# Optimization experiments

Hardware: AMD Instinct MI355X
Metric: run time of the kernel (lower is better)

## Reference

```python
import jax, jax.numpy as jnp
import numpy as np

E, D, F, K = 8, 1024, 4096, 2  # num_experts, embed_dim, intermediate_dim, top_k


def new_gelu(x):
    # NewGELUActivation: 0.5*x*(1+tanh(sqrt(2/pi)*(x+0.044715*x^3)))
    c = jnp.sqrt(2.0 / jnp.pi).astype(x.dtype)
    return 0.5 * x * (1.0 + jnp.tanh(c * (x + 0.044715 * x * x * x)))


def setup_inputs() -> dict:
    key = jax.random.key(0)
    ks = jax.random.split(key, 6)
    std = 0.02
    return {
        "hidden_states": jax.random.normal(ks[0], (4, 2048, D), dtype=jnp.float32),
        "gate_w": jax.random.normal(ks[1], (E, D), dtype=jnp.float32) * std,   # Linear(out=E,in=D), no bias
        "w_fc": jax.random.normal(ks[2], (E, F, D), dtype=jnp.float32) * std,  # per-expert c_fc weight [out,in]
        "b_fc": jnp.zeros((E, F), dtype=jnp.float32),
        "w_proj": jax.random.normal(ks[3], (E, D, F), dtype=jnp.float32) * std,
        "b_proj": jnp.zeros((E, D), dtype=jnp.float32),
    }


def reference(hidden_states, gate_w, w_fc, b_fc, w_proj, b_proj):
    B, S, _ = hidden_states.shape
    x = hidden_states.reshape(-1, D)                       # [T, D]
    T = x.shape[0]
    logits = x @ gate_w.T                                  # [T, E]
    topk_vals, topk_idx = jax.lax.top_k(logits, K)         # [T, K]
    topk_w = jax.nn.softmax(topk_vals, axis=-1)            # [T, K]
    # scatter top-k weights into a dense [T, E] sparse-weight matrix
    sparse_w = jnp.zeros((T, E), dtype=x.dtype).at[
        jnp.arange(T)[:, None], topk_idx
    ].set(topk_w)
    # per-expert dense MLP, combined with (mostly-zero) routing weights.
    # Mathematically identical to gather->MLP->scatter in the original
    # (dropout is identity in eval mode).
    out = jnp.zeros_like(x)
    for e in range(E):
        h = new_gelu(x @ w_fc[e].T + b_fc[e])              # [T, F]
        y = h @ w_proj[e].T + b_proj[e]                    # [T, D]
        out = out + y * sparse_w[:, e:e + 1]
    return out.reshape(B, S, D)
```

## Files before the change

### kernel.cpp

```cpp
#include <hip/hip_runtime.h>
#include <hip/hip_bf16.h>

#define E_ 8
#define D_ 1024
#define F_ 4096
#define K_ 2

typedef __attribute__((ext_vector_type(8))) short short8;
typedef __attribute__((ext_vector_type(4))) float f32x4;

__device__ __forceinline__ unsigned f2bf(float f){
  union { __hip_bfloat16 h; unsigned short u; } c;
  c.h = __float2bfloat16(f);
  return (unsigned)c.u;
}

__device__ __forceinline__ float bf2f(unsigned u){
  union { float f; unsigned u; } c;
  c.u = u << 16;
  return c.f;
}

__device__ __forceinline__ float gelu_f(float v){
  const float c0 = 0.7978845608028654f;
  float z = c0 * (v + 0.044715f * v * v * v);
  float e = __expf(2.0f * z);
  float t = 1.0f - 2.0f / (1.0f + e);
  return 0.5f * v * (1.0f + t);
}

__device__ __forceinline__ void gload16(const void* gsrc, void* ldst){
  __builtin_amdgcn_global_load_lds(
      (const __attribute__((address_space(1))) unsigned int*)gsrc,
      (__attribute__((address_space(3))) unsigned int*)ldst, 16, 0, 0);
}

__global__ void gate_kernel(const float* __restrict__ x, const float* __restrict__ gw,
                            int* __restrict__ tidx, float* __restrict__ tw, int T){
  int wid = threadIdx.x >> 6, lane = threadIdx.x & 63;
  int t = blockIdx.x * 4 + wid;
  if (t >= T) return;
  const float* xr = x + (size_t)t * D_;
  double acc[E_];
  #pragma unroll
  for (int e = 0; e < E_; ++e) acc[e] = 0.0;
  #pragma unroll
  for (int j = 0; j < 16; ++j){
    float xv = xr[j*64 + lane];
    #pragma unroll
    for (int e = 0; e < E_; ++e)
      acc[e] += (double)xv * (double)gw[e*D_ + j*64 + lane];
  }
  #pragma unroll
  for (int e = 0; e < E_; ++e){
    #pragma unroll
    for (int off = 32; off >= 1; off >>= 1)
      acc[e] += __shfl_xor(acc[e], off);
  }
  if (lane == 0){
    float l[E_];
    #pragma unroll
    for (int e = 0; e < E_; ++e) l[e] = (float)acc[e];
    int i0 = 0; float v0 = l[0];
    #pragma unroll
    for (int e = 1; e < E_; ++e) if (l[e] > v0){ v0 = l[e]; i0 = e; }
    int i1 = -1; float v1 = -1e30f;
    #pragma unroll
    for (int e = 0; e < E_; ++e) if (e != i0 && l[e] > v1){ v1 = l[e]; i1 = e; }
    float e1 = expf(v1 - v0);
    float s = 1.0f + e1;
    tidx[2*t] = i0; tidx[2*t+1] = i1;
    tw[2*t] = 1.0f / s; tw[2*t+1] = e1 / s;
  }
}

__global__ void slotscan_kernel(const int* __restrict__ tidx, int* __restrict__ counts,
                                int* __restrict__ tokSlot, int nAssign){
  __shared__ int cnt[256][E_];
  __shared__ int wtot[E_][4];
  __shared__ int ebase[E_];
  const int tid = threadIdx.x;
  const int lane = tid & 63, w = tid >> 6;
  const int per = (nAssign + 255) >> 8;
  const int base = tid * per;

  #pragma unroll
  for (int e = 0; e < E_; ++e) cnt[tid][e] = 0;
  for (int j = 0; j < per; ++j){
    int i = base + j;
    if (i < nAssign) cnt[tid][tidx[i]]++;
  }
  int excl[E_];
  #pragma unroll
  for (int e = 0; e < E_; ++e){
    int v = cnt[tid][e];
    int s = v;
    #pragma unroll
    for (int off = 1; off < 64; off <<= 1){
      int u = __shfl_up(s, off);
      if (lane >= off) s += u;
    }
    if (lane == 63) wtot[e][w] = s;
    excl[e] = s - v;
  }
  __syncthreads();
  if (tid == 0){
    int pre = 0;
    #pragma unroll
    for (int e = 0; e < E_; ++e){
      int tot = 0;
      #pragma unroll
      for (int ww = 0; ww < 4; ++ww){ int c = wtot[e][ww]; wtot[e][ww] = tot; tot += c; }
      counts[e] = tot;
      ebase[e] = pre;
      pre += (tot + 127) & ~127;
    }
  }
  __syncthreads();
  #pragma unroll
  for (int e = 0; e < E_; ++e)
    cnt[tid][e] = ebase[e] + wtot[e][w] + excl[e];
  for (int j = 0; j < per; ++j){
    int i = base + j;
    if (i < nAssign){
      int e = tidx[i];
      tokSlot[i] = cnt[tid][e]++;
    }
  }
}

__global__ void scatgath_kernel(const float* __restrict__ x,
                                const int* __restrict__ tokSlot,
                                __hip_bfloat16* __restrict__ Abuf){
  int t = blockIdx.x;
  int s0 = tokSlot[K_*t], s1 = tokSlot[K_*t + 1];
  const float4* src = reinterpret_cast<const float4*>(x + (size_t)t * D_) + threadIdx.x*2;
  float4 v0 = src[0], v1 = src[1];
  uint4 p;
  p.x = f2bf(v0.x) | (f2bf(v0.y) << 16);
  p.y = f2bf(v0.z) | (f2bf(v0.w) << 16);
  p.z = f2bf(v1.x) | (f2bf(v1.y) << 16);
  p.w = f2bf(v1.z) | (f2bf(v1.w) << 16);
  *(reinterpret_cast<uint4*>(reinterpret_cast<unsigned short*>(Abuf) + (size_t)s0*D_) + threadIdx.x) = p;
  *(reinterpret_cast<uint4*>(reinterpret_cast<unsigned short*>(Abuf) + (size_t)s1*D_) + threadIdx.x) = p;
}

__global__ void cvtw_kernel(const float* __restrict__ src, __hip_bfloat16* __restrict__ dst, int n4){
  int stride = gridDim.x * blockDim.x;
  for (int i = blockIdx.x * blockDim.x + threadIdx.x; i < n4; i += stride){
    float4 v = reinterpret_cast<const float4*>(src)[i];
    uint2 p;
    p.x = f2bf(v.x) | (f2bf(v.y) << 16);
    p.y = f2bf(v.z) | (f2bf(v.w) << 16);
    reinterpret_cast<uint2*>(dst)[i] = p;
  }
}

__global__ void combine_kernel(const unsigned short* __restrict__ Ybuf,
                               const int* __restrict__ tidx, const float* __restrict__ tw,
                               const int* __restrict__ tokSlot,
                               const float* __restrict__ bpj,
                               float* __restrict__ out){
  int t = blockIdx.x;
  int d = threadIdx.x * 4;
  int e0 = tidx[2*t], e1 = tidx[2*t+1];
  float w0 = tw[2*t], w1 = tw[2*t+1];
  int s0 = tokSlot[2*t], s1 = tokSlot[2*t+1];
  uint2 ya = *reinterpret_cast<const uint2*>(Ybuf + (size_t)s0*D_ + d);
  uint2 yb = *reinterpret_cast<const uint2*>(Ybuf + (size_t)s1*D_ + d);
  float4 b0 = *reinterpret_cast<const float4*>(bpj + (size_t)e0*D_ + d);
  float4 b1 = *reinterpret_cast<const float4*>(bpj + (size_t)e1*D_ + d);
  float4 r;
  r.x = w0*(bf2f(ya.x & 0xffffu) + b0.x) + w1*(bf2f(yb.x & 0xffffu) + b1.x);
  r.y = w0*(bf2f(ya.x >> 16)     + b0.y) + w1*(bf2f(yb.x >> 16)     + b1.y);
  r.z = w0*(bf2f(ya.y & 0xffffu) + b0.z) + w1*(bf2f(yb.y & 0xffffu) + b1.z);
  r.w = w0*(bf2f(ya.y >> 16)     + b0.w) + w1*(bf2f(yb.y >> 16)     + b1.w);
  *reinterpret_cast<float4*>(out + (size_t)t*D_ + d) = r;
}

template<bool WB16, bool PH1>
__global__ __launch_bounds__(256, 4) void gemm_kernel(
    const __hip_bfloat16* __restrict__ Abuf,
    const void* __restrict__ W,
    const float* __restrict__ bias,
    const int* __restrict__ counts,
    unsigned short* __restrict__ Out16)
{
  constexpr int KA = PH1 ? D_ : F_;
  constexpr int NT = PH1 ? F_ : D_;
  constexpr int NK = KA / 64;
  constexpr int NX = NT / 128;

  __shared__ char sA[128*128];
  __shared__ char sB[128*128];

  int pre[E_]; int total = 0;
  #pragma unroll
  for (int i = 0; i < E_; ++i){ pre[i] = total; total += (counts[i] + 127) & ~127; }

  int q = gridDim.x >> 3;
  int wgid = (blockIdx.x & 7) * q + (blockIdx.x >> 3);
  int yt = wgid / NX, xt = wgid - yt * NX;
  int rowBase = yt * 128;
  if (rowBase >= total) return;
  int e = 0;
  #pragma unroll
  for (int i = 1; i < E_; ++i) if (rowBase >= pre[i]) e = i;
  int nBase = xt * 128;

  const int tid = threadIdx.x;
  const int wid = tid >> 6, lane = tid & 63;
  const int lr = lane & 15, lg = lane >> 4;
  const int wr = wid >> 1, wc = wid & 1;

  const unsigned short* Wb = (const unsigned short*)W;
  const float* Wf = (const float*)W;
  const size_t Wrow0 = (size_t)e * NT + nBase;

  f32x4 acc[4][4];
  #pragma unroll
  for (int m = 0; m < 4; ++m)
    #pragma unroll
    for (int n = 0; n < 4; ++n) acc[m][n] = (f32x4){0.f,0.f,0.f,0.f};

  for (int kt = 0; kt < NK; ++kt){
    int k0 = kt * 64;
    #pragma unroll
    for (int i = 0; i < 4; ++i){
      int flat = i*4096 + wid*1024 + lane*16;
      int row  = flat >> 7;
      int colb = flat & 127;
      int scol = colb ^ ((row & 7) << 4);
      const char* src = (const char*)(Abuf + (size_t)(rowBase + row) * KA + k0) + scol;
      gload16(src, sA + i*4096 + wid*1024);
    }
    if constexpr (WB16){
      #pragma unroll
      for (int i = 0; i < 4; ++i){
        int flat = i*4096 + wid*1024 + lane*16;
        int row  = flat >> 7;
        int colb = flat & 127;
        int scol = colb ^ ((row & 7) << 4);
        const char* src = (const char*)(Wb + (Wrow0 + row) * KA + k0) + scol;
        gload16(src, sB + i*4096 + wid*1024);
      }
    } else {
      #pragma unroll
      for (int i = 0; i < 8; ++i){
        int f4  = i*256 + tid;
        int row = f4 >> 4;
        int c4  = f4 & 15;
        float4 v = *reinterpret_cast<const float4*>(Wf + (Wrow0 + row) * KA + k0 + c4*4);
        uint2 p;
        p.x = f2bf(v.x) | (f2bf(v.y) << 16);
        p.y = f2bf(v.z) | (f2bf(v.w) << 16);
        int byte = row*128 + c4*8;
        *reinterpret_cast<uint2*>(sB + (byte ^ ((row & 7) << 4))) = p;
      }
    }
    __syncthreads();
    #pragma unroll
    for (int ks = 0; ks < 2; ++ks){
      short8 a[4], b[4];
      #pragma unroll
      for (int m = 0; m < 4; ++m){
        int row = wr*64 + m*16 + lr;
        a[m] = *reinterpret_cast<const short8*>(sA + row*128 + ((ks*64 + lg*16) ^ ((row & 7) << 4)));
      }
      #pragma unroll
      for (int n = 0; n < 4; ++n){
        int row = wc*64 + n*16 + lr;
        b[n] = *reinterpret_cast<const short8*>(sB + row*128 + ((ks*64 + lg*16) ^ ((row & 7) << 4)));
      }
      #pragma unroll
      for (int m = 0; m < 4; ++m)
        #pragma unroll
        for (int n = 0; n < 4; ++n)
          acc[m][n] = __builtin_amdgcn_mfma_f32_16x16x32_bf16(b[n], a[m], acc[m][n], 0, 0, 0);
    }
    __syncthreads();
  }

  int colBase = nBase + wc*64;
  if constexpr (PH1){
    #pragma unroll
    for (int n = 0; n < 4; ++n){
      int gc = colBase + n*16 + lg*4;
      float4 b4 = *reinterpret_cast<const float4*>(bias + (size_t)e*F_ + gc);
      #pragma unroll
      for (int m = 0; m < 4; ++m){
        int grow = rowBase + wr*64 + m*16 + lr;
        uint2 p;
        p.x = f2bf(gelu_f(acc[m][n][0] + b4.x)) | (f2bf(gelu_f(acc[m][n][1] + b4.y)) << 16);
        p.y = f2bf(gelu_f(acc[m][n][2] + b4.z)) | (f2bf(gelu_f(acc[m][n][3] + b4.w)) << 16);
        *reinterpret_cast<uint2*>(Out16 + (size_t)grow * F_ + gc) = p;
      }
    }
  } else {
    #pragma unroll
    for (int n = 0; n < 4; ++n){
      int gc = colBase + n*16 + lg*4;
      #pragma unroll
      for (int m = 0; m < 4; ++m){
        int grow = rowBase + wr*64 + m*16 + lr;
        uint2 p;
        p.x = f2bf(acc[m][n][0]) | (f2bf(acc[m][n][1]) << 16);
        p.y = f2bf(acc[m][n][2]) | (f2bf(acc[m][n][3]) << 16);
        *reinterpret_cast<uint2*>(Out16 + (size_t)grow * D_ + gc) = p;
      }
    }
  }
}

extern "C" void kernel_launch(void* const* d_in, const int* in_sizes, int n_in,
                              void* d_out, int out_size, void* d_ws, size_t ws_size,
                              hipStream_t stream){
  const float* x   = (const float*)d_in[0];
  const float* gw  = (const float*)d_in[1];
  const float* wfc = (const float*)d_in[2];
  const float* bfc = (const float*)d_in[3];
  const float* wpj = (const float*)d_in[4];
  const float* bpj = (const float*)d_in[5];
  float* out = (float*)d_out;

  int T = in_sizes[0] / D_;
  int nAssign = T * K_;
  int nSlotsMax = nAssign + E_ * 128;
  int rowTiles = nSlotsMax / 128;

  char* ws = (char*)d_ws;
  size_t o = 0;
  int*   tidx    = (int*)(ws + o); o += (size_t)nAssign * 4;
  float* tw      = (float*)(ws + o); o += (size_t)nAssign * 4;
  int*   counts  = (int*)(ws + o); o += 256;
  int*   tokSlot = (int*)(ws + o); o += (size_t)nAssign * 4;
  o = (o + 255) & ~(size_t)255;

  size_t abytes = (size_t)nSlotsMax * D_ * 2;
  size_t hbytes = (size_t)nSlotsMax * F_ * 2;
  size_t wbytes = (size_t)E_ * F_ * D_ * 2;

  __hip_bfloat16* Abuf = (__hip_bfloat16*)(ws + o); o += abytes;
  __hip_bfloat16* Hbuf = (__hip_bfloat16*)(ws + o); o += hbytes;
  size_t o_w = o;
  __hip_bfloat16* wA = (__hip_bfloat16*)(ws + o_w);
  __hip_bfloat16* wB = (__hip_bfloat16*)(ws + o_w + wbytes);

  bool newPath = (ws_size >= o_w + 2*wbytes);
  bool midPath = (ws_size >= o_w + wbytes);

  int n4 = E_ * F_ * D_ / 4;
  int nwg1 = (F_/128) * rowTiles;
  int nwg2 = (D_/128) * rowTiles;
  unsigned short* Ybuf = (unsigned short*)Abuf;

  gate_kernel<<<(T + 3)/4, 256, 0, stream>>>(x, gw, tidx, tw, T);
  slotscan_kernel<<<1, 256, 0, stream>>>(tidx, counts, tokSlot, nAssign);
  scatgath_kernel<<<T, 128, 0, stream>>>(x, tokSlot, Abuf);

  if (newPath){
    cvtw_kernel<<<2048, 256, 0, stream>>>(wfc, wA, n4);
    cvtw_kernel<<<2048, 256, 0, stream>>>(wpj, wB, n4);
    gemm_kernel<true, true><<<nwg1, 256, 0, stream>>>(
        Abuf, (const void*)wA, bfc, counts, (unsigned short*)Hbuf);
    gemm_kernel<true, false><<<nwg2, 256, 0, stream>>>(
        Hbuf, (const void*)wB, bpj, counts, Ybuf);
  } else if (midPath){
    cvtw_kernel<<<2048, 256, 0, stream>>>(wfc, wA, n4);
    gemm_kernel<true, true><<<nwg1, 256, 0, stream>>>(
        Abuf, (const void*)wA, bfc, counts, (unsigned short*)Hbuf);
    cvtw_kernel<<<2048, 256, 0, stream>>>(wpj, wA, n4);
    gemm_kernel<true, false><<<nwg2, 256, 0, stream>>>(
        Hbuf, (const void*)wA, bpj, counts, Ybuf);
  } else {
    gemm_kernel<false, true><<<nwg1, 256, 0, stream>>>(
        Abuf, (const void*)wfc, bfc, counts, (unsigned short*)Hbuf);
    gemm_kernel<false, false><<<nwg2, 256, 0, stream>>>(
        Hbuf, (const void*)wpj, bpj, counts, Ybuf);
  }
  combine_kernel<<<T, 256, 0, stream>>>(Ybuf, tidx, tw, tokSlot, bpj, out);
}
```

Baseline: 524.7 us.

## Add 256x256-tile pipelined GEMM kernel for the expert FC phase

Adds a new 512-thread GEMM kernel with 256x256 output tiles, double-buffered swizzled LDS staging, split-phase prefetch interleaved with MFMA groups, and raised wave priority during the MFMA blocks. It is used for the first (D->F) expert GEMM in the bf16-weight paths. Expert slot padding grows from 128 to 256 rows so the larger tiles align to expert boundaries. The larger tiles give more data reuse per global load, at the cost of more padded rows, more registers and lower occupancy.

```diff
diff --git a/kernel.cpp b/kernel.cpp
--- a/kernel.cpp
+++ b/kernel.cpp
@@ -5,6 +5,7 @@
 #define D_ 1024
 #define F_ 4096
 #define K_ 2
+#define ALIGN_ 256
 
 typedef __attribute__((ext_vector_type(8))) short short8;
 typedef __attribute__((ext_vector_type(4))) float f32x4;
@@ -113,7 +114,7 @@
       for (int ww = 0; ww < 4; ++ww){ int c = wtot[e][ww]; wtot[e][ww] = tot; tot += c; }
       counts[e] = tot;
       ebase[e] = pre;
-      pre += (tot + 127) & ~127;
+      pre += (tot + (ALIGN_-1)) & ~(ALIGN_-1);
     }
   }
   __syncthreads();
@@ -178,6 +179,205 @@
   *reinterpret_cast<float4*>(out + (size_t)t*D_ + d) = r;
 }
 
+
+__device__ __forceinline__ short8 frag(const char* plane, int r, int ks, int lg){
+  int cb = ks*64 + lg*16;
+  return *reinterpret_cast<const short8*>(plane + r*128 + (cb ^ ((r & 7) << 4)));
+}
+
+__device__ __forceinline__ void stage_half(const unsigned short* g, int ldk,
+                                           char* plane, int tid){
+  #pragma unroll
+  for (int i = 0; i < 2; ++i){
+    int flat = i*8192 + tid*16;
+    int r = flat >> 7;
+    int cb = flat & 127;
+    int scb = cb ^ ((r & 7) << 4);
+    gload16((const char*)(g + (size_t)r * ldk) + scb,
+            plane + i*8192 + (tid & ~63)*16);
+  }
+}
+
+template<bool PH1>
+__global__ __launch_bounds__(512, 2) void gemm256_kernel(
+    const __hip_bfloat16* __restrict__ Abuf,
+    const __hip_bfloat16* __restrict__ W,
+    const float* __restrict__ bias,
+    const int* __restrict__ counts,
+    unsigned short* __restrict__ Out16)
+{
+  constexpr int KA  = PH1 ? D_ : F_;
+  constexpr int NT  = PH1 ? F_ : D_;
+  constexpr int NKT = KA / 64;
+  constexpr int NX  = NT / 256;
+
+  __shared__ __align__(16) char sA[2][2][16384];
+  __shared__ __align__(16) char sB[2][2][16384];
+
+  int pre[E_]; int total = 0;
+  #pragma unroll
+  for (int i = 0; i < E_; ++i){ pre[i] = total; total += (counts[i] + (ALIGN_-1)) & ~(ALIGN_-1); }
+
+  int q = gridDim.x >> 3;
+  int wgid = (blockIdx.x & 7) * q + (blockIdx.x >> 3);
+  int NYt = gridDim.x / NX;
+  int xt = wgid / NYt;
+  int yt = wgid - xt * NYt;
+  int rowBase = yt * 256;
+  if (rowBase >= total) return;
+  int e = 0;
+  #pragma unroll
+  for (int i = 1; i < E_; ++i) if (rowBase >= pre[i]) e = i;
+  int nBase = xt * 256;
+
+  const int tid = threadIdx.x;
+  const int lane = tid & 63, wid = tid >> 6;
+  const int lr = lane & 15, lg = lane >> 4;
+  const int wr = wid >> 2, wc = wid & 3;
+
+  const unsigned short* AbR = (const unsigned short*)Abuf + (size_t)rowBase * KA;
+  const unsigned short* BbR = (const unsigned short*)W + ((size_t)e * NT + nBase) * KA;
+
+  f32x4 acc[8][4];
+  #pragma unroll
+  for (int m = 0; m < 8; ++m)
+    #pragma unroll
+    for (int n = 0; n < 4; ++n) acc[m][n] = (f32x4){0.f,0.f,0.f,0.f};
+
+  stage_half(AbR,                      KA, sA[0][0], tid);
+  stage_half(AbR + (size_t)128*KA,     KA, sA[0][1], tid);
+  stage_half(BbR,                      KA, sB[0][0], tid);
+  stage_half(BbR + (size_t)128*KA,     KA, sB[0][1], tid);
+  stage_half(BbR + 64,                 KA, sB[1][0], tid);
+  stage_half(BbR + (size_t)128*KA + 64,KA, sB[1][1], tid);
+  stage_half(AbR + 64,                 KA, sA[1][0], tid);
+  asm volatile("s_waitcnt vmcnt(6)" ::: "memory");
+  __builtin_amdgcn_s_barrier();
+
+  const char* pAh[2] = { sA[0][wr], sA[1][wr] };
+  const char* pBh[2] = { sB[0][wc>>1], sB[1][wc>>1] };
+  const int rB0 = (wc & 1) * 64;
+
+  for (int t = 0; t < NKT; ++t){
+    const int buf = t & 1;
+    const char* pA = pAh[buf];
+    const char* pB = pBh[buf];
+    const int k1 = (t + 1) * 64, k2 = (t + 2) * 64;
+    const bool s1 = (t + 1 < NKT), s2 = (t + 2 < NKT);
+
+    short8 b[4][2], a0[2][2];
+    #pragma unroll
+    for (int n = 0; n < 4; ++n)
+      #pragma unroll
+      for (int ks = 0; ks < 2; ++ks)
+        b[n][ks] = frag(pB, rB0 + n*16 + lr, ks, lg);
+    #pragma unroll
+    for (int m = 0; m < 2; ++m)
+      #pragma unroll
+      for (int ks = 0; ks < 2; ++ks)
+        a0[m][ks] = frag(pA, m*16 + lr, ks, lg);
+    if (s1) stage_half(AbR + (size_t)128*KA + k1, KA, sA[buf^1][1], tid);
+    __builtin_amdgcn_s_barrier();
+    asm volatile("s_waitcnt lgkmcnt(0)" ::: "memory");
+    __builtin_amdgcn_sched_barrier(0);
+    __builtin_amdgcn_s_setprio(1);
+    #pragma unroll
+    for (int m = 0; m < 2; ++m)
+      #pragma unroll
+      for (int n = 0; n < 4; ++n)
+        #pragma unroll
+        for (int ks = 0; ks < 2; ++ks)
+          acc[m][n] = __builtin_amdgcn_mfma_f32_16x16x32_bf16(b[n][ks], a0[m][ks], acc[m][n], 0, 0, 0);
+    __builtin_amdgcn_s_setprio(0);
+    __builtin_amdgcn_s_barrier();
+
+    short8 a1[4][2];
+    #pragma unroll
+    for (int m = 0; m < 4; ++m)
+      #pragma unroll
+      for (int ks = 0; ks < 2; ++ks)
+        a1[m][ks] = frag(pA, (m+2)*16 + lr, ks, lg);
+    if (s2) stage_half(BbR + k2, KA, sB[buf][0], tid);
+    __builtin_amdgcn_s_barrier();
+    asm volatile("s_waitcnt lgkmcnt(0)" ::: "memory");
+    __builtin_amdgcn_sched_barrier(0);
+    __builtin_amdgcn_s_setprio(1);
+    #pragma unroll
+    for (int m = 0; m < 2; ++m)
+      #pragma unroll
+      for (int n = 0; n < 4; ++n)
+        #pragma unroll
+        for (int ks = 0; ks < 2; ++ks)
+          acc[m+2][n] = __builtin_amdgcn_mfma_f32_16x16x32_bf16(b[n][ks], a1[m][ks], acc[m+2][n], 0, 0, 0);
+    __builtin_amdgcn_s_setprio(0);
+    __builtin_amdgcn_s_barrier();
+
+    short8 a2[2][2];
+    #pragma unroll
+    for (int m = 0; m < 2; ++m)
+      #pragma unroll
+      for (int ks = 0; ks < 2; ++ks)
+        a2[m][ks] = frag(pA, (m+6)*16 + lr, ks, lg);
+    if (s2) stage_half(BbR + (size_t)128*KA + k2, KA, sB[buf][1], tid);
+    __builtin_amdgcn_s_barrier();
+    asm volatile("s_waitcnt lgkmcnt(0)" ::: "memory");
+    __builtin_amdgcn_sched_barrier(0);
+    __builtin_amdgcn_s_setprio(1);
+    #pragma unroll
+    for (int m = 0; m < 2; ++m)
+      #pragma unroll
+      for (int n = 0; n < 4; ++n)
+        #pragma unroll
+        for (int ks = 0; ks < 2; ++ks)
+          acc[m+4][n] = __builtin_amdgcn_mfma_f32_16x16x32_bf16(b[n][ks], a1[m+2][ks], acc[m+4][n], 0, 0, 0);
+    __builtin_amdgcn_s_setprio(0);
+    __builtin_amdgcn_s_barrier();
+
+    if (s2){
+      stage_half(AbR + k2, KA, sA[buf][0], tid);
+      asm volatile("s_waitcnt vmcnt(6)" ::: "memory");
+    } else {
+      asm volatile("s_waitcnt vmcnt(0)" ::: "memory");
+    }
+    __builtin_amdgcn_s_barrier();
+    __builtin_amdgcn_s_setprio(1);
+    #pragma unroll
+    for (int m = 0; m < 2; ++m)
+      #pragma unroll
+      for (int n = 0; n < 4; ++n)
+        #pragma unroll
+        for (int ks = 0; ks < 2; ++ks)
+          acc[m+6][n] = __builtin_amdgcn_mfma_f32_16x16x32_bf16(b[n][ks], a2[m][ks], acc[m+6][n], 0, 0, 0);
+    __builtin_amdgcn_s_setprio(0);
+    __builtin_amdgcn_s_barrier();
+  }
+
+  #pragma unroll
+  for (int n = 0; n < 4; ++n){
+    int gc = nBase + wc*64 + n*16 + lg*4;
+    if constexpr (PH1){
+      float4 b4 = *reinterpret_cast<const float4*>(bias + (size_t)e*F_ + gc);
+      #pragma unroll
+      for (int m = 0; m < 8; ++m){
+        int gr = rowBase + wr*128 + m*16 + lr;
+        uint2 p;
+        p.x = f2bf(gelu_f(acc[m][n][0] + b4.x)) | (f2bf(gelu_f(acc[m][n][1] + b4.y)) << 16);
+        p.y = f2bf(gelu_f(acc[m][n][2] + b4.z)) | (f2bf(gelu_f(acc[m][n][3] + b4.w)) << 16);
+        *reinterpret_cast<uint2*>(Out16 + (size_t)gr * F_ + gc) = p;
+      }
+    } else {
+      #pragma unroll
+      for (int m = 0; m < 8; ++m){
+        int gr = rowBase + wr*128 + m*16 + lr;
+        uint2 p;
+        p.x = f2bf(acc[m][n][0]) | (f2bf(acc[m][n][1]) << 16);
+        p.y = f2bf(acc[m][n][2]) | (f2bf(acc[m][n][3]) << 16);
+        *reinterpret_cast<uint2*>(Out16 + (size_t)gr * D_ + gc) = p;
+      }
+    }
+  }
+}
+
 template<bool WB16, bool PH1>
 __global__ __launch_bounds__(256, 4) void gemm_kernel(
     const __hip_bfloat16* __restrict__ Abuf,
@@ -196,11 +396,11 @@
 
   int pre[E_]; int total = 0;
   #pragma unroll
-  for (int i = 0; i < E_; ++i){ pre[i] = total; total += (counts[i] + 127) & ~127; }
+  for (int i = 0; i < E_; ++i){ pre[i] = total; total += (counts[i] + (ALIGN_-1)) & ~(ALIGN_-1); }
 
   int q = gridDim.x >> 3;
   int wgid = (blockIdx.x & 7) * q + (blockIdx.x >> 3);
-  int yt = wgid / NX, xt = wgid - yt * NX;
+  int yt = wgid / NX, xt = wgid - yt*NX;
   int rowBase = yt * 128;
   if (rowBase >= total) return;
   int e = 0;
@@ -289,11 +489,11 @@
       float4 b4 = *reinterpret_cast<const float4*>(bias + (size_t)e*F_ + gc);
       #pragma unroll
       for (int m = 0; m < 4; ++m){
-        int grow = rowBase + wr*64 + m*16 + lr;
+        int gr = rowBase + wr*64 + m*16 + lr;
         uint2 p;
         p.x = f2bf(gelu_f(acc[m][n][0] + b4.x)) | (f2bf(gelu_f(acc[m][n][1] + b4.y)) << 16);
         p.y = f2bf(gelu_f(acc[m][n][2] + b4.z)) | (f2bf(gelu_f(acc[m][n][3] + b4.w)) << 16);
-        *reinterpret_cast<uint2*>(Out16 + (size_t)grow * F_ + gc) = p;
+        *reinterpret_cast<uint2*>(Out16 + (size_t)gr * F_ + gc) = p;
       }
     }
   } else {
@@ -302,11 +502,11 @@
       int gc = colBase + n*16 + lg*4;
       #pragma unroll
       for (int m = 0; m < 4; ++m){
-        int grow = rowBase + wr*64 + m*16 + lr;
+        int gr = rowBase + wr*64 + m*16 + lr;
         uint2 p;
         p.x = f2bf(acc[m][n][0]) | (f2bf(acc[m][n][1]) << 16);
         p.y = f2bf(acc[m][n][2]) | (f2bf(acc[m][n][3]) << 16);
-        *reinterpret_cast<uint2*>(Out16 + (size_t)grow * D_ + gc) = p;
+        *reinterpret_cast<uint2*>(Out16 + (size_t)gr * D_ + gc) = p;
       }
     }
   }
@@ -325,8 +525,9 @@
 
   int T = in_sizes[0] / D_;
   int nAssign = T * K_;
-  int nSlotsMax = nAssign + E_ * 128;
-  int rowTiles = nSlotsMax / 128;
+  int nSlotsMax = nAssign + E_ * ALIGN_;
+  int rowTiles128 = nSlotsMax / 128;
+  int rowTiles256 = nSlotsMax / 256;
 
   char* ws = (char*)d_ws;
   size_t o = 0;
@@ -350,8 +551,9 @@
   bool midPath = (ws_size >= o_w + wbytes);
 
   int n4 = E_ * F_ * D_ / 4;
-  int nwg1 = (F_/128) * rowTiles;
-  int nwg2 = (D_/128) * rowTiles;
+  int nwg1_256 = (F_/256) * rowTiles256;
+  int nwg2_128 = (D_/128) * rowTiles128;
+  int nwg1_128 = (F_/128) * rowTiles128;
   unsigned short* Ybuf = (unsigned short*)Abuf;
 
   gate_kernel<<<(T + 3)/4, 256, 0, stream>>>(x, gw, tidx, tw, T);
@@ -361,21 +563,21 @@
   if (newPath){
     cvtw_kernel<<<2048, 256, 0, stream>>>(wfc, wA, n4);
     cvtw_kernel<<<2048, 256, 0, stream>>>(wpj, wB, n4);
-    gemm_kernel<true, true><<<nwg1, 256, 0, stream>>>(
-        Abuf, (const void*)wA, bfc, counts, (unsigned short*)Hbuf);
-    gemm_kernel<true, false><<<nwg2, 256, 0, stream>>>(
+    gemm256_kernel<true><<<nwg1_256, 512, 0, stream>>>(
+        Abuf, wA, bfc, counts, (unsigned short*)Hbuf);
+    gemm_kernel<true, false><<<nwg2_128, 256, 0, stream>>>(
         Hbuf, (const void*)wB, bpj, counts, Ybuf);
   } else if (midPath){
     cvtw_kernel<<<2048, 256, 0, stream>>>(wfc, wA, n4);
-    gemm_kernel<true, true><<<nwg1, 256, 0, stream>>>(
-        Abuf, (const void*)wA, bfc, counts, (unsigned short*)Hbuf);
+    gemm256_kernel<true><<<nwg1_256, 512, 0, stream>>>(
+        Abuf, wA, bfc, counts, (unsigned short*)Hbuf);
     cvtw_kernel<<<2048, 256, 0, stream>>>(wpj, wA, n4);
-    gemm_kernel<true, false><<<nwg2, 256, 0, stream>>>(
+    gemm_kernel<true, false><<<nwg2_128, 256, 0, stream>>>(
         Hbuf, (const void*)wA, bpj, counts, Ybuf);
   } else {
-    gemm_kernel<false, true><<<nwg1, 256, 0, stream>>>(
+    gemm_kernel<false, true><<<nwg1_128, 256, 0, stream>>>(
         Abuf, (const void*)wfc, bfc, counts, (unsigned short*)Hbuf);
-    gemm_kernel<false, false><<<nwg2, 256, 0, stream>>>(
+    gemm_kernel<false, false><<<nwg2_128, 256, 0, stream>>>(
         Hbuf, (const void*)wpj, bpj, counts, Ybuf);
   }
   combine_kernel<<<T, 256, 0, stream>>>(Ybuf, tidx, tw, tokSlot, bpj, out);
```

Result: slower. 708.7 us (+35.1%).
